# Kernel tuning notes

Measured on AMD Instinct MI355X. Metric: run time of the kernel, lower is better.

Reference implementation:

```python
import jax, jax.numpy as jnp
import numpy as np

EMBED = 1024
HEADS = 16

def setup_inputs() -> dict:
    key = jax.random.key(0)
    ks = jax.random.split(key, 6)
    N, S = 1, 4096
    half = EMBED // 2
    x = jax.random.normal(ks[0], (N, S, EMBED), dtype=jnp.float32)
    Wq = jax.random.normal(ks[1], (half, half), dtype=jnp.float32) * 0.02
    Wk = jax.random.normal(ks[2], (half, half), dtype=jnp.float32) * 0.02
    Wv = jax.random.normal(ks[3], (half, half), dtype=jnp.float32) * 0.02
    Wo = jax.random.normal(ks[4], (EMBED, half), dtype=jnp.float32) * 0.02
    bo = jnp.zeros((EMBED,), dtype=jnp.float32)
    return {"x": x, "Wq": Wq, "Wk": Wk, "Wv": Wv, "Wo": Wo, "bo": bo}

def reference(x, Wq, Wk, Wv, Wo, bo):
    N, S, E = x.shape
    H = HEADS
    Dh = (E // 2) // H                 # per-head dim of the half-width projections (32)
    scale = float(E // H) ** 0.5       # original scales by head_dim = embed/heads = 64
    left = x[..., : E // 2]            # only the left chunk feeds attention in the source
    # torch Linear: y = x @ W.T (no bias)
    q = (left @ Wq.T).reshape(N, S, H, Dh)
    k = (left @ Wk.T).reshape(N, S, H, Dh)
    v = (left @ Wv.T).reshape(N, S, H, Dh)
    energy = jnp.einsum('nqhd,nkhd->nqkh', q, k)          # [N,S,S,H] full score tensor
    att = jax.nn.softmax(energy / scale, axis=2)          # softmax over key axis
    out = jnp.einsum('nqkh,nkhd->nqhd', att, v)           # [N,S,H,Dh]
    out = out.reshape(N, S, E // 2)
    return out @ Wo.T + bo                                # fc_out: half -> embed
```

## Files before the change

kernel.cpp:

```cpp
#include <hip/hip_runtime.h>
#include <stdint.h>


#define SEQ    4096
#define DMODEL 1024
#define DHALF  512
#define NH     16
#define DH     32

typedef __attribute__((ext_vector_type(4))) float facc4;
typedef __attribute__((ext_vector_type(8))) short bfrag8;

#define MFMA_BF16(a, b, c) __builtin_amdgcn_mfma_f32_16x16x32_bf16((a), (b), (c), 0, 0, 0)

static __device__ __forceinline__ uint16_t f2b(float x) {
    uint32_t u = __float_as_uint(x);
    return (uint16_t)((u + 0x7FFFu + ((u >> 16) & 1u)) >> 16);
}
static __device__ __forceinline__ float b2f(uint16_t b) {
    return __uint_as_float(((uint32_t)b) << 16);
}

static __device__ __forceinline__ bfrag8 cvt8perm(float4 a, float4 b) {
    uint32_t u0 = __float_as_uint(a.x) + 0x8000u, u1 = __float_as_uint(a.y) + 0x8000u;
    uint32_t u2 = __float_as_uint(a.z) + 0x8000u, u3 = __float_as_uint(a.w) + 0x8000u;
    uint32_t u4 = __float_as_uint(b.x) + 0x8000u, u5 = __float_as_uint(b.y) + 0x8000u;
    uint32_t u6 = __float_as_uint(b.z) + 0x8000u, u7 = __float_as_uint(b.w) + 0x8000u;
    union { uint32_t w[4]; bfrag8 r; } u;
    u.w[0] = __builtin_amdgcn_perm(u1, u0, 0x07060302u);
    u.w[1] = __builtin_amdgcn_perm(u3, u2, 0x07060302u);
    u.w[2] = __builtin_amdgcn_perm(u5, u4, 0x07060302u);
    u.w[3] = __builtin_amdgcn_perm(u7, u6, 0x07060302u);
    return u.r;
}

__global__ __launch_bounds__(256) void convert_w(
    const float* __restrict__ Wq, const float* __restrict__ Wk,
    const float* __restrict__ Wv, const float* __restrict__ Wo,
    uint16_t* __restrict__ q, uint16_t* __restrict__ k,
    uint16_t* __restrict__ v, uint16_t* __restrict__ o)
{
    int zz = blockIdx.x;
    const float* src; uint16_t* dst; size_t off;
    if      (zz < 128) { src = Wq; dst = q; off = (size_t)zz * 2048; }
    else if (zz < 256) { src = Wk; dst = k; off = (size_t)(zz - 128) * 2048; }
    else if (zz < 384) { src = Wv; dst = v; off = (size_t)(zz - 256) * 2048; }
    else               { src = Wo; dst = o; off = (size_t)(zz - 384) * 2048; }
    size_t i = off + (size_t)threadIdx.x * 8;
    float4 a = *(const float4*)&src[i];
    float4 b = *(const float4*)&src[i + 4];
    *(bfrag8*)&dst[i] = cvt8perm(a, b);
}

template <int AF32>
__device__ __forceinline__ void gemm128T(
    const void* __restrict__ A, int lda,
    const uint16_t* __restrict__ B, int ldb,
    void* __restrict__ C, int ldc, int cF32,
    const float* __restrict__ bias, float scale,
    int Kd, int m0, int n0)
{
    __shared__ __align__(16) uint16_t As[2][128 * 40];
    __shared__ __align__(16) uint16_t Bs[2][128 * 40];

    const int tid  = threadIdx.x;
    const int lane = tid & 63;
    const int wv   = tid >> 6;
    const int lo   = lane & 15;
    const int quad = lane >> 4;
    const int srow = tid >> 2;
    const int skq  = (tid & 3) * 8;
    const int rb   = (wv >> 1) * 64;
    const int cb   = (wv & 1) * 64;

    const facc4 ZACC = {0.f, 0.f, 0.f, 0.f};
    facc4 acc[4][4];
#pragma unroll
    for (int i = 0; i < 4; ++i)
#pragma unroll
        for (int j = 0; j < 4; ++j) acc[i][j] = ZACC;

    const float*    fA0 = AF32 ? &((const float*)A)[(size_t)(m0 + srow) * lda + skq] : nullptr;
    const float*    fA1 = AF32 ? &((const float*)A)[(size_t)(m0 + srow + 64) * lda + skq] : nullptr;
    const uint16_t* hA0 = AF32 ? nullptr : &((const uint16_t*)A)[(size_t)(m0 + srow) * lda + skq];
    const uint16_t* hA1 = AF32 ? nullptr : &((const uint16_t*)A)[(size_t)(m0 + srow + 64) * lda + skq];
    const uint16_t* pB0 = &B[(size_t)(n0 + srow) * ldb + skq];
    const uint16_t* pB1 = &B[(size_t)(n0 + srow + 64) * ldb + skq];

    bfrag8 ra0, ra1;
    float4 f0a, f0b, f1a, f1b;
    if (AF32) {
        f0a = *(const float4*)fA0; f0b = *(const float4*)(fA0 + 4);
        f1a = *(const float4*)fA1; f1b = *(const float4*)(fA1 + 4);
    } else {
        ra0 = *(const bfrag8*)hA0;
        ra1 = *(const bfrag8*)hA1;
    }
    bfrag8 rb0 = *(const bfrag8*)pB0;
    bfrag8 rb1 = *(const bfrag8*)pB1;

    if (AF32) {
        *(bfrag8*)&As[0][srow * 40 + skq]        = cvt8perm(f0a, f0b);
        *(bfrag8*)&As[0][(srow + 64) * 40 + skq] = cvt8perm(f1a, f1b);
    } else {
        *(bfrag8*)&As[0][srow * 40 + skq]        = ra0;
        *(bfrag8*)&As[0][(srow + 64) * 40 + skq] = ra1;
    }
    *(bfrag8*)&Bs[0][srow * 40 + skq]        = rb0;
    *(bfrag8*)&Bs[0][(srow + 64) * 40 + skq] = rb1;
    __syncthreads();

    int p = 0;
    for (int kt = 0; kt < Kd; kt += 32) {
        const bool more = (kt + 32 < Kd);
        if (more) {
            if (AF32) {
                f0a = *(const float4*)(fA0 + kt + 32); f0b = *(const float4*)(fA0 + kt + 36);
                f1a = *(const float4*)(fA1 + kt + 32); f1b = *(const float4*)(fA1 + kt + 36);
            } else {
                ra0 = *(const bfrag8*)(hA0 + kt + 32);
                ra1 = *(const bfrag8*)(hA1 + kt + 32);
            }
            rb0 = *(const bfrag8*)(pB0 + kt + 32);
            rb1 = *(const bfrag8*)(pB1 + kt + 32);
        }

        bfrag8 af[4], bf[4];
#pragma unroll
        for (int i = 0; i < 4; ++i) {
            af[i] = *(const bfrag8*)&As[p][(rb + i * 16 + lo) * 40 + quad * 8];
            bf[i] = *(const bfrag8*)&Bs[p][(cb + i * 16 + lo) * 40 + quad * 8];
        }
#pragma unroll
        for (int i = 0; i < 4; ++i)
#pragma unroll
            for (int j = 0; j < 4; ++j)
                acc[i][j] = MFMA_BF16(af[i], bf[j], acc[i][j]);

        if (more) {
            if (AF32) {
                *(bfrag8*)&As[1 - p][srow * 40 + skq]        = cvt8perm(f0a, f0b);
                *(bfrag8*)&As[1 - p][(srow + 64) * 40 + skq] = cvt8perm(f1a, f1b);
            } else {
                *(bfrag8*)&As[1 - p][srow * 40 + skq]        = ra0;
                *(bfrag8*)&As[1 - p][(srow + 64) * 40 + skq] = ra1;
            }
            *(bfrag8*)&Bs[1 - p][srow * 40 + skq]        = rb0;
            *(bfrag8*)&Bs[1 - p][(srow + 64) * 40 + skq] = rb1;
            __syncthreads();
            p ^= 1;
        }
    }

#pragma unroll
    for (int j = 0; j < 4; ++j) {
        int col  = n0 + cb + j * 16 + lo;
        float bv = bias ? bias[col] : 0.f;
#pragma unroll
        for (int i = 0; i < 4; ++i) {
#pragma unroll
            for (int r = 0; r < 4; ++r) {
                int row = m0 + rb + i * 16 + quad * 4 + r;
                float v = acc[i][j][r] * scale + bv;
                if (cF32) ((float*)C)[(size_t)row * ldc + col] = v;
                else      ((uint16_t*)C)[(size_t)row * ldc + col] = f2b(v);
            }
        }
    }
}

#define SC_Q (0.125f * 1.4426950408889634f)

__global__ __launch_bounds__(256, 2) void qkv_kernel(
    const float* __restrict__ x,
    const uint16_t* __restrict__ Wqb, const uint16_t* __restrict__ Wkb,
    const uint16_t* __restrict__ Wvb,
    uint16_t* __restrict__ Q, uint16_t* __restrict__ K, uint16_t* __restrict__ V)
{
    const int z = blockIdx.z;
    const uint16_t* W = (z == 0) ? Wqb : (z == 1) ? Wkb : Wvb;
    uint16_t* Out     = (z == 0) ? Q   : (z == 1) ? K   : V;
    float scale       = (z == 0) ? SC_Q : 1.0f;
    gemm128T<1>(x, DMODEL, W, DHALF, Out, DHALF, 0, nullptr, scale, DHALF,
                blockIdx.y * 128, blockIdx.x * 128);
}

__global__ __launch_bounds__(256, 2) void outproj_kernel(
    const uint16_t* __restrict__ O, const uint16_t* __restrict__ Wob,
    const float* __restrict__ bo, float* __restrict__ Y)
{
    gemm128T<0>(O, DHALF, Wob, DHALF, Y, DMODEL, 1, bo, 1.0f, DHALF,
                blockIdx.y * 128, blockIdx.x * 128);
}

__global__ __launch_bounds__(256) void attn_kernel(
    const uint16_t* __restrict__ Q, const uint16_t* __restrict__ Kb,
    const uint16_t* __restrict__ Vb, uint16_t* __restrict__ Op,
    float* __restrict__ lbuf, int kspan)
{
    __shared__ __align__(16) uint16_t Ks[2][64 * 40];
    __shared__ __align__(16) uint16_t Vt[2][32 * 64];

    const int tid  = threadIdx.x;
    const int lane = tid & 63;
    const int wv   = tid >> 6;
    const int lo   = lane & 15;
    const int quad = lane >> 4;
    const int h    = blockIdx.y;
    const int q0   = blockIdx.x * 64;
    const int sp   = blockIdx.z;
    const int srow = tid >> 2;
    const int skq  = (tid & 3) * 8;

    const facc4 ZACC = {0.f, 0.f, 0.f, 0.f};

    const bfrag8 qf = *(const bfrag8*)&Q[(size_t)(q0 + wv * 16 + lo) * DHALF + h * DH + quad * 8];

    bfrag8 ones;
#pragma unroll
    for (int j = 0; j < 8; ++j) ones[j] = (short)0x3F80;

    int vt_w[8];
    {
        int pb = ((srow >> 5) << 2) | ((srow >> 2) & 3);
        int pw = (((srow >> 4) & 1) << 2) | (srow & 3);
#pragma unroll
        for (int j = 0; j < 8; ++j) {
            int d  = skq + j;
            int Rd = ((d & 7) + 2 * (d >> 3)) & 7;
            vt_w[j] = d * 64 + (((pb + Rd) & 7) << 3) + pw;
        }
    }
    int vt_r[2][2];
#pragma unroll
    for (int dt = 0; dt < 2; ++dt) {
        int d  = dt * 16 + lo;
        int Rd = ((d & 7) + 2 * (d >> 3)) & 7;
#pragma unroll
        for (int c = 0; c < 2; ++c)
            vt_r[c][dt] = d * 64 + ((((c * 4 + quad) + Rd) & 7) << 3);
    }
    const int ks_r = lo * 40 + quad * 8;

    const uint16_t* pK = &Kb[(size_t)srow * DHALF + h * DH + skq];
    const uint16_t* pV = &Vb[(size_t)srow * DHALF + h * DH + skq];

    facc4 oacc[2], oaccL;
    oacc[0] = ZACC; oacc[1] = ZACC; oaccL = ZACC;

    const int kb0  = sp * kspan;
    const int kend = kb0 + kspan;

    float4 kreg = *(const float4*)(pK + (size_t)kb0 * DHALF);
    float4 vreg = *(const float4*)(pV + (size_t)kb0 * DHALF);

    *(float4*)&Ks[0][srow * 40 + skq] = kreg;
    {
        const uint16_t* vp = (const uint16_t*)&vreg;
#pragma unroll
        for (int j = 0; j < 8; ++j) Vt[0][vt_w[j]] = vp[j];
    }
    __syncthreads();

    int p = 0;
    for (int kb = kb0; kb < kend; kb += 64) {
        const bool more = (kb + 64 < kend);
        if (more) {
            kreg = *(const float4*)(pK + (size_t)(kb + 64) * DHALF);
            vreg = *(const float4*)(pV + (size_t)(kb + 64) * DHALF);
        }

        uint2 w[4];
#pragma unroll
        for (int t = 0; t < 4; ++t) {
            bfrag8 kf = *(const bfrag8*)&Ks[p][t * 640 + ks_r];
            facc4 s = MFMA_BF16(kf, qf, ZACC);
            float p0 = __builtin_amdgcn_exp2f(s[0]);
            float p1 = __builtin_amdgcn_exp2f(s[1]);
            float p2 = __builtin_amdgcn_exp2f(s[2]);
            float p3 = __builtin_amdgcn_exp2f(s[3]);
            uint32_t u0 = __float_as_uint(p0) + 0x8000u;
            uint32_t u1 = __float_as_uint(p1) + 0x8000u;
            uint32_t u2 = __float_as_uint(p2) + 0x8000u;
            uint32_t u3 = __float_as_uint(p3) + 0x8000u;
            w[t].x = __builtin_amdgcn_perm(u1, u0, 0x07060302u);
            w[t].y = __builtin_amdgcn_perm(u3, u2, 0x07060302u);
        }

        union PU { uint2 u2[2]; bfrag8 f; };
        PU pu0, pu1;
        pu0.u2[0] = w[0]; pu0.u2[1] = w[1];
        pu1.u2[0] = w[2]; pu1.u2[1] = w[3];

#pragma unroll
        for (int c = 0; c < 2; ++c) {
            bfrag8 pf = c ? pu1.f : pu0.f;
#pragma unroll
            for (int dt = 0; dt < 2; ++dt) {
                bfrag8 vf = *(const bfrag8*)&Vt[p][vt_r[c][dt]];
                oacc[dt] = MFMA_BF16(pf, vf, oacc[dt]);
            }
            oaccL = MFMA_BF16(pf, ones, oaccL);
        }

        if (more) {
            *(float4*)&Ks[p ^ 1][srow * 40 + skq] = kreg;
            const uint16_t* vp = (const uint16_t*)&vreg;
#pragma unroll
            for (int j = 0; j < 8; ++j) Vt[p ^ 1][vt_w[j]] = vp[j];
            __syncthreads();
            p ^= 1;
        }
    }

    if (lo == 0) {
#pragma unroll
        for (int r = 0; r < 4; ++r)
            lbuf[((size_t)sp * NH + h) * SEQ + q0 + wv * 16 + quad * 4 + r] = oaccL[r];
    }

    uint16_t* Od = Op + (size_t)sp * SEQ * DHALF;
#pragma unroll
    for (int r = 0; r < 4; ++r) {
        int row = q0 + wv * 16 + quad * 4 + r;
        Od[(size_t)row * DHALF + h * DH + lo]      = f2b(oacc[0][r]);
        Od[(size_t)row * DHALF + h * DH + 16 + lo] = f2b(oacc[1][r]);
    }
}

__global__ __launch_bounds__(256) void combine_kernel(
    const uint16_t* __restrict__ Op, const float* __restrict__ lbuf,
    uint16_t* __restrict__ O, int ns)
{
    int t   = blockIdx.x * 256 + threadIdx.x;
    int row = t >> 6;
    int cb  = (t & 63) << 3;
    int h   = cb >> 5;
    float l = 0.f;
    float acc[8] = {0.f, 0.f, 0.f, 0.f, 0.f, 0.f, 0.f, 0.f};
    for (int sp = 0; sp < ns; ++sp) {
        l += lbuf[((size_t)sp * NH + h) * SEQ + row];
        bfrag8 a = *(const bfrag8*)&Op[(size_t)sp * SEQ * DHALF + (size_t)row * DHALF + cb];
#pragma unroll
        for (int j = 0; j < 8; ++j) acc[j] += b2f((uint16_t)a[j]);
    }
    float inv = 1.0f / l;
    bfrag8 o;
#pragma unroll
    for (int j = 0; j < 8; ++j) o[j] = (short)f2b(acc[j] * inv);
    *(bfrag8*)&O[(size_t)row * DHALF + cb] = o;
}

extern "C" void kernel_launch(void* const* d_in, const int* in_sizes, int n_in,
                              void* d_out, int out_size, void* d_ws, size_t ws_size,
                              hipStream_t stream)
{
    const float* x  = (const float*)d_in[0];
    const float* Wq = (const float*)d_in[1];
    const float* Wk = (const float*)d_in[2];
    const float* Wv = (const float*)d_in[3];
    const float* Wo = (const float*)d_in[4];
    const float* bo = (const float*)d_in[5];

    size_t fixed_e = 3 * (size_t)DHALF * DHALF + (size_t)DMODEL * DHALF
                   + 4 * (size_t)SEQ * DHALF;
    size_t need4 = (fixed_e + 4 * (size_t)SEQ * DHALF) * 2
                 + 4 * (size_t)NH * SEQ * 4;
    const int ns = (ws_size >= need4) ? 4 : 2;

    uint16_t* Wqb = (uint16_t*)d_ws;
    uint16_t* Wkb = Wqb + (size_t)DHALF * DHALF;
    uint16_t* Wvb = Wkb + (size_t)DHALF * DHALF;
    uint16_t* Wob = Wvb + (size_t)DHALF * DHALF;
    uint16_t* Q   = Wob + (size_t)DMODEL * DHALF;
    uint16_t* K   = Q + (size_t)SEQ * DHALF;
    uint16_t* V   = K + (size_t)SEQ * DHALF;
    uint16_t* O   = V + (size_t)SEQ * DHALF;
    uint16_t* Op  = O + (size_t)SEQ * DHALF;
    float*  lbuf  = (float*)(Op + (size_t)ns * SEQ * DHALF);

    convert_w<<<640, 256, 0, stream>>>(Wq, Wk, Wv, Wo, Wqb, Wkb, Wvb, Wob);
    qkv_kernel<<<dim3(DHALF / 128, SEQ / 128, 3), 256, 0, stream>>>(
        x, Wqb, Wkb, Wvb, Q, K, V);
    attn_kernel<<<dim3(SEQ / 64, NH, ns), 256, 0, stream>>>(Q, K, V, Op, lbuf, SEQ / ns);
    combine_kernel<<<1024, 256, 0, stream>>>(Op, lbuf, O, ns);
    outproj_kernel<<<dim3(DMODEL / 128, SEQ / 128), 256, 0, stream>>>(
        O, Wob, bo, (float*)d_out);
}
```

Baseline: 189.0 us.

## Process two query sub-tiles per wave to reuse K/V tiles in attention

Each attention block now covers 128 queries instead of 64, with every wave holding two 16-row Q fragments that share each K and V fragment read from LDS. This halves the K/V global loads and LDS staging per query and the number of blocks. The double-buffer loop is manually unrolled by two with macros, which removes the buffer-index toggle. In exchange each thread uses more accumulator registers, the grid is half as large, and the loop assumes an even number of 64-key tiles per split.

Measured after the change: 176.5 us. 6.6% less time.

```diff
diff --git a/kernel.cpp b/kernel.cpp
--- a/kernel.cpp
+++ b/kernel.cpp
@@ -207,14 +207,16 @@
     const int lo   = lane & 15;
     const int quad = lane >> 4;
     const int h    = blockIdx.y;
-    const int q0   = blockIdx.x * 64;
+    const int q0   = blockIdx.x * 128;
     const int sp   = blockIdx.z;
     const int srow = tid >> 2;
     const int skq  = (tid & 3) * 8;
 
     const facc4 ZACC = {0.f, 0.f, 0.f, 0.f};
 
-    const bfrag8 qf = *(const bfrag8*)&Q[(size_t)(q0 + wv * 16 + lo) * DHALF + h * DH + quad * 8];
+    bfrag8 qf[2];
+    qf[0] = *(const bfrag8*)&Q[(size_t)(q0 + wv * 32 + lo) * DHALF + h * DH + quad * 8];
+    qf[1] = *(const bfrag8*)&Q[(size_t)(q0 + wv * 32 + 16 + lo) * DHALF + h * DH + quad * 8];
 
     bfrag8 ones;
 #pragma unroll
@@ -242,89 +244,110 @@
     }
     const int ks_r = lo * 40 + quad * 8;
 
-    const uint16_t* pK = &Kb[(size_t)srow * DHALF + h * DH + skq];
-    const uint16_t* pV = &Vb[(size_t)srow * DHALF + h * DH + skq];
-
-    facc4 oacc[2], oaccL;
-    oacc[0] = ZACC; oacc[1] = ZACC; oaccL = ZACC;
-
-    const int kb0  = sp * kspan;
-    const int kend = kb0 + kspan;
-
-    float4 kreg = *(const float4*)(pK + (size_t)kb0 * DHALF);
-    float4 vreg = *(const float4*)(pV + (size_t)kb0 * DHALF);
-
-    *(float4*)&Ks[0][srow * 40 + skq] = kreg;
-    {
-        const uint16_t* vp = (const uint16_t*)&vreg;
-#pragma unroll
-        for (int j = 0; j < 8; ++j) Vt[0][vt_w[j]] = vp[j];
-    }
+    const uint16_t* kp = &Kb[(size_t)(sp * kspan + srow) * DHALF + h * DH + skq];
+    const uint16_t* vp = &Vb[(size_t)(sp * kspan + srow) * DHALF + h * DH + skq];
+
+    facc4 oacc[2][2], oaccL[2];
+    oacc[0][0] = ZACC; oacc[0][1] = ZACC;
+    oacc[1][0] = ZACC; oacc[1][1] = ZACC;
+    oaccL[0] = ZACC; oaccL[1] = ZACC;
+
+    float4 kreg = *(const float4*)kp;
+    float4 vreg = *(const float4*)vp;
+    kp += 64 * DHALF;
+    vp += 64 * DHALF;
+
+#define STAGE(BUF) do {                                                       \
+        *(float4*)&Ks[BUF][srow * 40 + skq] = kreg;                           \
+        const uint16_t* vsp = (const uint16_t*)&vreg;                         \
+        _Pragma("unroll")                                                     \
+        for (int j = 0; j < 8; ++j) Vt[BUF][vt_w[j]] = vsp[j];                \
+    } while (0)
+
+#define TILE(BUF) do {                                                        \
+        uint2 w0[4], w1[4];                                                   \
+        _Pragma("unroll")                                                     \
+        for (int t4 = 0; t4 < 4; ++t4) {                                      \
+            bfrag8 kf = *(const bfrag8*)&Ks[BUF][t4 * 640 + ks_r];            \
+            facc4 s0 = MFMA_BF16(kf, qf[0], ZACC);                            \
+            facc4 s1 = MFMA_BF16(kf, qf[1], ZACC);                            \
+            uint32_t a0 = __float_as_uint(__builtin_amdgcn_exp2f(s0[0])) + 0x8000u; \
+            uint32_t a1 = __float_as_uint(__builtin_amdgcn_exp2f(s0[1])) + 0x8000u; \
+            uint32_t a2 = __float_as_uint(__builtin_amdgcn_exp2f(s0[2])) + 0x8000u; \
+            uint32_t a3 = __float_as_uint(__builtin_amdgcn_exp2f(s0[3])) + 0x8000u; \
+            w0[t4].x = __builtin_amdgcn_perm(a1, a0, 0x07060302u);            \
+            w0[t4].y = __builtin_amdgcn_perm(a3, a2, 0x07060302u);            \
+            uint32_t b0 = __float_as_uint(__builtin_amdgcn_exp2f(s1[0])) + 0x8000u; \
+            uint32_t b1 = __float_as_uint(__builtin_amdgcn_exp2f(s1[1])) + 0x8000u; \
+            uint32_t b2 = __float_as_uint(__builtin_amdgcn_exp2f(s1[2])) + 0x8000u; \
+            uint32_t b3 = __float_as_uint(__builtin_amdgcn_exp2f(s1[3])) + 0x8000u; \
+            w1[t4].x = __builtin_amdgcn_perm(b1, b0, 0x07060302u);            \
+            w1[t4].y = __builtin_amdgcn_perm(b3, b2, 0x07060302u);            \
+        }                                                                     \
+        union PU { uint2 u2[2]; bfrag8 f; } pu;                               \
+        bfrag8 pf0[2], pf1[2];                                                \
+        pu.u2[0] = w0[0]; pu.u2[1] = w0[1]; pf0[0] = pu.f;                    \
+        pu.u2[0] = w0[2]; pu.u2[1] = w0[3]; pf0[1] = pu.f;                    \
+        pu.u2[0] = w1[0]; pu.u2[1] = w1[1]; pf1[0] = pu.f;                    \
+        pu.u2[0] = w1[2]; pu.u2[1] = w1[3]; pf1[1] = pu.f;                    \
+        _Pragma("unroll")                                                     \
+        for (int c = 0; c < 2; ++c) {                                         \
+            _Pragma("unroll")                                                 \
+            for (int dt = 0; dt < 2; ++dt) {                                  \
+                bfrag8 vf = *(const bfrag8*)&Vt[BUF][vt_r[c][dt]];            \
+                oacc[0][dt] = MFMA_BF16(pf0[c], vf, oacc[0][dt]);             \
+                oacc[1][dt] = MFMA_BF16(pf1[c], vf, oacc[1][dt]);             \
+            }                                                                 \
+            oaccL[0] = MFMA_BF16(pf0[c], ones, oaccL[0]);                     \
+            oaccL[1] = MFMA_BF16(pf1[c], ones, oaccL[1]);                     \
+        }                                                                     \
+    } while (0)
+
+    STAGE(0);
     __syncthreads();
 
-    int p = 0;
-    for (int kb = kb0; kb < kend; kb += 64) {
-        const bool more = (kb + 64 < kend);
+    const int nt = kspan >> 6;
+    for (int t = 0; t < nt; t += 2) {
+        kreg = *(const float4*)kp;
+        vreg = *(const float4*)vp;
+        kp += 64 * DHALF; vp += 64 * DHALF;
+        TILE(0);
+        STAGE(1);
+        __syncthreads();
+
+        const bool more = (t + 2 < nt);
         if (more) {
-            kreg = *(const float4*)(pK + (size_t)(kb + 64) * DHALF);
-            vreg = *(const float4*)(pV + (size_t)(kb + 64) * DHALF);
-        }
-
-        uint2 w[4];
-#pragma unroll
-        for (int t = 0; t < 4; ++t) {
-            bfrag8 kf = *(const bfrag8*)&Ks[p][t * 640 + ks_r];
-            facc4 s = MFMA_BF16(kf, qf, ZACC);
-            float p0 = __builtin_amdgcn_exp2f(s[0]);
-            float p1 = __builtin_amdgcn_exp2f(s[1]);
-            float p2 = __builtin_amdgcn_exp2f(s[2]);
-            float p3 = __builtin_amdgcn_exp2f(s[3]);
-            uint32_t u0 = __float_as_uint(p0) + 0x8000u;
-            uint32_t u1 = __float_as_uint(p1) + 0x8000u;
-            uint32_t u2 = __float_as_uint(p2) + 0x8000u;
-            uint32_t u3 = __float_as_uint(p3) + 0x8000u;
-            w[t].x = __builtin_amdgcn_perm(u1, u0, 0x07060302u);
-            w[t].y = __builtin_amdgcn_perm(u3, u2, 0x07060302u);
-        }
-
-        union PU { uint2 u2[2]; bfrag8 f; };
-        PU pu0, pu1;
-        pu0.u2[0] = w[0]; pu0.u2[1] = w[1];
-        pu1.u2[0] = w[2]; pu1.u2[1] = w[3];
-
-#pragma unroll
-        for (int c = 0; c < 2; ++c) {
-            bfrag8 pf = c ? pu1.f : pu0.f;
-#pragma unroll
-            for (int dt = 0; dt < 2; ++dt) {
-                bfrag8 vf = *(const bfrag8*)&Vt[p][vt_r[c][dt]];
-                oacc[dt] = MFMA_BF16(pf, vf, oacc[dt]);
-            }
-            oaccL = MFMA_BF16(pf, ones, oaccL);
-        }
-
+            kreg = *(const float4*)kp;
+            vreg = *(const float4*)vp;
+            kp += 64 * DHALF; vp += 64 * DHALF;
+        }
+        TILE(1);
         if (more) {
-            *(float4*)&Ks[p ^ 1][srow * 40 + skq] = kreg;
-            const uint16_t* vp = (const uint16_t*)&vreg;
-#pragma unroll
-            for (int j = 0; j < 8; ++j) Vt[p ^ 1][vt_w[j]] = vp[j];
+            STAGE(0);
             __syncthreads();
-            p ^= 1;
-        }
-    }
+        }
+    }
+#undef STAGE
+#undef TILE
 
     if (lo == 0) {
 #pragma unroll
-        for (int r = 0; r < 4; ++r)
-            lbuf[((size_t)sp * NH + h) * SEQ + q0 + wv * 16 + quad * 4 + r] = oaccL[r];
+        for (int g = 0; g < 2; ++g)
+#pragma unroll
+            for (int r = 0; r < 4; ++r)
+                lbuf[((size_t)sp * NH + h) * SEQ + q0 + wv * 32 + g * 16 + quad * 4 + r] =
+                    oaccL[g][r];
     }
 
     uint16_t* Od = Op + (size_t)sp * SEQ * DHALF;
 #pragma unroll
-    for (int r = 0; r < 4; ++r) {
-        int row = q0 + wv * 16 + quad * 4 + r;
-        Od[(size_t)row * DHALF + h * DH + lo]      = f2b(oacc[0][r]);
-        Od[(size_t)row * DHALF + h * DH + 16 + lo] = f2b(oacc[1][r]);
+    for (int g = 0; g < 2; ++g) {
+#pragma unroll
+        for (int r = 0; r < 4; ++r) {
+            int row = q0 + wv * 32 + g * 16 + quad * 4 + r;
+            Od[(size_t)row * DHALF + h * DH + lo]      = f2b(oacc[g][0][r]);
+            Od[(size_t)row * DHALF + h * DH + 16 + lo] = f2b(oacc[g][1][r]);
+        }
     }
 }
 
@@ -382,7 +405,7 @@
     convert_w<<<640, 256, 0, stream>>>(Wq, Wk, Wv, Wo, Wqb, Wkb, Wvb, Wob);
     qkv_kernel<<<dim3(DHALF / 128, SEQ / 128, 3), 256, 0, stream>>>(
         x, Wqb, Wkb, Wvb, Q, K, V);
-    attn_kernel<<<dim3(SEQ / 64, NH, ns), 256, 0, stream>>>(Q, K, V, Op, lbuf, SEQ / ns);
+    attn_kernel<<<dim3(SEQ / 128, NH, ns), 256, 0, stream>>>(Q, K, V, Op, lbuf, SEQ / ns);
     combine_kernel<<<1024, 256, 0, stream>>>(Op, lbuf, O, ns);
     outproj_kernel<<<dim3(DMODEL / 128, SEQ / 128), 256, 0, stream>>>(
         O, Wob, bo, (float*)d_out);
```
